# Performance work log

Hardware: AMD Instinct MI355X
Metric: run time of the kernel (lower is better)

Reference implementation:

```python
import jax, jax.numpy as jnp
import numpy as np

QLEN, MLEN, BSZ = 1024, 1024, 2
D_MODEL, N_HEAD, D_HEAD, D_INNER = 1024, 16, 64, 4096
KLEN = QLEN + MLEN
RLEN = KLEN + QLEN
EPS = 1e-12
SCALE = 1.0 / np.sqrt(D_HEAD).astype(np.float32)
STD = 0.02


def gelu(x):
    # OpenAI-GPT tanh-approx gelu used by XLNet
    return 0.5 * x * (1.0 + jnp.tanh(np.sqrt(2.0 / np.pi) * (x + 0.044715 * x ** 3)))


def layer_norm(x, g, b):
    m = jnp.mean(x, axis=-1, keepdims=True)
    v = jnp.mean((x - m) ** 2, axis=-1, keepdims=True)
    return (x - m) * jax.lax.rsqrt(v + EPS) * g + b


def rel_shift(x, klen):
    # x: [qlen, rlen, bsz, n_head] -> [qlen, klen, bsz, n_head]
    q, r, b, n = x.shape
    x = jnp.reshape(x, (r, q, b, n))[1:]
    x = jnp.reshape(x, (q, r - 1, b, n))[:, :klen]
    return x


def setup_inputs() -> dict:
    key = jax.random.key(0)
    ks = jax.random.split(key, 16)
    h = jax.random.normal(ks[0], (QLEN, BSZ, D_MODEL), jnp.float32)
    mems = jax.random.normal(ks[1], (MLEN, BSZ, D_MODEL), jnp.float32)
    r = jax.random.normal(ks[2], (RLEN, BSZ, D_MODEL), jnp.float32)
    # segment one-hot: 1 if query and key segments differ (XLNet convention)
    qseg = jax.random.randint(ks[3], (QLEN, BSZ), 0, 2)
    kseg = jax.random.randint(ks[4], (KLEN, BSZ), 0, 2)
    seg_mat = jax.nn.one_hot((qseg[:, None, :] != kseg[None, :, :]).astype(jnp.int32), 2, dtype=jnp.float32)  # [q,k,b,2]
    # causal mask with mems: query i may attend to key j <= i + MLEN
    i = jnp.arange(QLEN)[:, None]
    j = jnp.arange(KLEN)[None, :]
    attn_mask = (j > i + MLEN).astype(jnp.float32)[:, :, None, None]  # [q,k,1,1]
    wq = jax.random.normal(ks[5], (D_MODEL, N_HEAD, D_HEAD), jnp.float32) * STD
    wk = jax.random.normal(ks[6], (D_MODEL, N_HEAD, D_HEAD), jnp.float32) * STD
    wv = jax.random.normal(ks[7], (D_MODEL, N_HEAD, D_HEAD), jnp.float32) * STD
    wo = jax.random.normal(ks[8], (D_MODEL, N_HEAD, D_HEAD), jnp.float32) * STD
    wr = jax.random.normal(ks[9], (D_MODEL, N_HEAD, D_HEAD), jnp.float32) * STD
    r_w_bias = jnp.zeros((N_HEAD, D_HEAD), jnp.float32)
    r_r_bias = jnp.zeros((N_HEAD, D_HEAD), jnp.float32)
    r_s_bias = jnp.zeros((N_HEAD, D_HEAD), jnp.float32)
    seg_embed = jax.random.normal(ks[10], (2, N_HEAD, D_HEAD), jnp.float32) * STD
    ln_attn_g = jnp.ones((D_MODEL,), jnp.float32)
    ln_attn_b = jnp.zeros((D_MODEL,), jnp.float32)
    w1 = jax.random.normal(ks[11], (D_MODEL, D_INNER), jnp.float32) * STD
    b1 = jnp.zeros((D_INNER,), jnp.float32)
    w2 = jax.random.normal(ks[12], (D_INNER, D_MODEL), jnp.float32) * STD
    b2 = jnp.zeros((D_MODEL,), jnp.float32)
    ln_ff_g = jnp.ones((D_MODEL,), jnp.float32)
    ln_ff_b = jnp.zeros((D_MODEL,), jnp.float32)
    return dict(h=h, mems=mems, r=r, seg_mat=seg_mat, attn_mask=attn_mask,
                wq=wq, wk=wk, wv=wv, wo=wo, wr=wr,
                r_w_bias=r_w_bias, r_r_bias=r_r_bias, r_s_bias=r_s_bias, seg_embed=seg_embed,
                ln_attn_g=ln_attn_g, ln_attn_b=ln_attn_b,
                w1=w1, b1=b1, w2=w2, b2=b2, ln_ff_g=ln_ff_g, ln_ff_b=ln_ff_b)


def reference(h, mems, r, seg_mat, attn_mask, wq, wk, wv, wo, wr,
              r_w_bias, r_r_bias, r_s_bias, seg_embed,
              ln_attn_g, ln_attn_b, w1, b1, w2, b2, ln_ff_g, ln_ff_b):
    # content-stream XLNet relative attention (g=None path) + FFN
    cat = jnp.concatenate([mems, h], axis=0)            # [klen,b,h]
    q_h = jnp.einsum('ibh,hnd->ibnd', h, wq)
    k_h = jnp.einsum('ibh,hnd->ibnd', cat, wk)
    v_h = jnp.einsum('ibh,hnd->ibnd', cat, wv)
    k_r = jnp.einsum('ibh,hnd->ibnd', r, wr)
    ac = jnp.einsum('ibnd,jbnd->ijbn', q_h + r_w_bias, k_h)
    bd = jnp.einsum('ibnd,jbnd->ijbn', q_h + r_r_bias, k_r)
    bd = rel_shift(bd, KLEN)
    ef = jnp.einsum('ibnd,snd->ibns', q_h + r_s_bias, seg_embed)
    ef = jnp.einsum('ijbs,ibns->ijbn', seg_mat, ef)
    attn_score = (ac + bd + ef) * SCALE - 1e30 * attn_mask
    attn_prob = jax.nn.softmax(attn_score, axis=1)
    attn_vec = jnp.einsum('ijbn,jbnd->ibnd', attn_prob, v_h)
    attn_out = jnp.einsum('ibnd,hnd->ibh', attn_vec, wo) + h
    out_h = layer_norm(attn_out, ln_attn_g, ln_attn_b)
    ff = gelu(out_h @ w1 + b1) @ w2 + b2
    return layer_norm(ff + out_h, ln_ff_g, ln_ff_b)
```

## Files before the change

### kernel.cpp

```cpp
#include <hip/hip_runtime.h>
#include <hip/hip_bf16.h>


#define QLEN 1024
#define MLEN 1024
#define DM 1024
#define NH 16
#define DH 64
#define DI 4096
#define KLEN 2048
#define RLEN 3072

typedef __attribute__((ext_vector_type(8))) short s16x8;
typedef __attribute__((ext_vector_type(4))) float f32x4;
typedef unsigned short us;

__device__ __forceinline__ float bf2f(us u) {
    union { unsigned int i; float f; } x; x.i = ((unsigned int)u) << 16; return x.f;
}
__device__ __forceinline__ us f2bf(float f) {
    union { float f; unsigned int i; } x; x.f = f;
    return (us)((x.i + 0x7fffu + ((x.i >> 16) & 1u)) >> 16);
}
__device__ __forceinline__ void gload16(const void* g, void* lds) {
    __builtin_amdgcn_global_load_lds(
        (const __attribute__((address_space(1))) unsigned int*)g,
        (__attribute__((address_space(3))) unsigned int*)lds, 16, 0, 0);
}

template<bool ISMAX>
__device__ __forceinline__ float block_reduce(float v, float* red, int t) {
    #pragma unroll
    for (int off = 32; off > 0; off >>= 1) {
        float o = __shfl_down(v, off);
        v = ISMAX ? fmaxf(v, o) : (v + o);
    }
    if ((t & 63) == 0) red[t >> 6] = v;
    __syncthreads();
    if (t == 0) {
        float s = red[0];
        #pragma unroll
        for (int w = 1; w < 4; ++w) s = ISMAX ? fmaxf(s, red[w]) : (s + red[w]);
        red[4] = s;
    }
    __syncthreads();
    return red[4];
}

__global__ __launch_bounds__(256) void prep_k(
    const float* __restrict__ mems, const float* __restrict__ h,
    const float* __restrict__ r, const float* __restrict__ wo,
    const float* __restrict__ wq, const float* __restrict__ wk,
    const float* __restrict__ wv, const float* __restrict__ wr,
    const float* __restrict__ w1, const float* __restrict__ w2,
    const float* __restrict__ seg,
    us* __restrict__ cat_bf, us* __restrict__ r_bf, us* __restrict__ wo_b,
    us* __restrict__ wqkv_t, us* __restrict__ wr_t,
    us* __restrict__ w1_t, us* __restrict__ w2_t, us* __restrict__ ksb)
{
    __shared__ us tbuf[64][65];
    int bid = blockIdx.x;
    const int tid = threadIdx.x;
    if (bid < 5632) {
        int t = bid * 256 + tid;
        const float* src; us* dst; int off;
        if (t < 262144)       { src = mems; dst = cat_bf;           off = t; }
        else if (t < 524288)  { src = h;    dst = cat_bf + 2097152; off = t - 262144; }
        else if (t < 1310720) { src = r;    dst = r_bf;             off = t - 524288; }
        else                  { src = wo;   dst = wo_b;             off = t - 1310720; }
        const float4* p = (const float4*)src + 2 * (size_t)off;
        float4 a = p[0], b = p[1];
        us o[8] = { f2bf(a.x), f2bf(a.y), f2bf(a.z), f2bf(a.w),
                    f2bf(b.x), f2bf(b.y), f2bf(b.z), f2bf(b.w) };
        *((uint4*)dst + off) = *(const uint4*)o;
        return;
    }
    bid -= 5632;
    if (bid >= 3072) {
        int t = (bid - 3072) * 256 + tid;
        int bb = t >> 11, j = t & 2047;
        ksb[t] = f2bf(seg[(size_t)j * 4 + bb * 2 + 1]);
        return;
    }
    const float* in; us* out; int R, C, c0, r0;
    if (bid < 1024) {
        int z = bid >> 8, u = bid & 255;
        in  = (z == 0) ? wq : (z == 1) ? wk : (z == 2) ? wv : wr;
        out = (z < 3) ? (wqkv_t + (size_t)z * 1048576) : wr_t;
        R = 1024; C = 1024; c0 = (u & 15) * 64; r0 = (u >> 4) * 64;
    } else if (bid < 2048) {
        int u = bid - 1024;
        in = w1; out = w1_t; R = 1024; C = 4096;
        c0 = (u & 63) * 64; r0 = (u >> 6) * 64;
    } else {
        int u = bid - 2048;
        in = w2; out = w2_t; R = 4096; C = 1024;
        c0 = (u & 15) * 64; r0 = (u >> 4) * 64;
    }
    #pragma unroll
    for (int u = 0; u < 16; ++u) {
        int idx = tid + 256 * u;
        int rr = idx >> 6, cc = idx & 63;
        tbuf[cc][rr] = f2bf(in[(size_t)(r0 + rr) * C + c0 + cc]);
    }
    __syncthreads();
    #pragma unroll
    for (int u = 0; u < 16; ++u) {
        int idx = tid + 256 * u;
        int rr = idx >> 6, cc = idx & 63;
        out[(size_t)(c0 + rr) * R + r0 + cc] = tbuf[rr][cc];
    }
}

__device__ __forceinline__ int offe(int r, int c) {
    return ((r >> 4) * 2 + (c >> 5)) * 512 + (r & 15) * 32 + ((c & 31) ^ ((r & 8) ? 16 : 0));
}

template<int EPI>
__device__ __forceinline__ void gemm8_core(
    const us* __restrict__ A, const us* __restrict__ Bt,
    const float* __restrict__ bias, void* __restrict__ Cout,
    int N, int K, int kbeg, size_t zoff, bool zfirst,
    int bx, int by, us* __restrict__ As8, us* __restrict__ Bs8)
{
    const int tid = threadIdx.x;
    const int w = tid >> 6, l = tid & 63;
    const int lm = l & 15, lg = l >> 4;
    const int wm = w >> 2, wn = w & 3;
    const int m0 = by * 256, n0 = bx * 256;

    int srow[2], scol[2];
    #pragma unroll
    for (int u = 0; u < 2; ++u) {
        int sub = w * 2 + u;
        srow[u] = (sub >> 1) * 16 + (l >> 2);
        scol[u] = (sub & 1) * 32 + (((l & 3) * 8) ^ ((l & 32) ? 16 : 0));
    }

    auto stagePart = [&](int kt1, int P, int db) {
        const us* src = (P < 2) ? (A + (size_t)(m0 + P * 128) * K)
                                : (Bt + (size_t)(n0 + (P - 2) * 128) * K);
        us* dst = ((P < 2) ? As8 : Bs8) + (db * 2 + (P & 1)) * 8192;
        int kc = kbeg + kt1 * 64;
        #pragma unroll
        for (int u = 0; u < 2; ++u)
            gload16(src + (size_t)srow[u] * K + kc + scol[u], dst + (w * 2 + u) * 512);
    };

    f32x4 acc[8][4] = {};
    s16x8 rA0[4][2], rA1[4][2], rB[2][2];

    stagePart(0, 0, 0); stagePart(0, 1, 0); stagePart(0, 2, 0); stagePart(0, 3, 0);

    for (int kt = 0; kt < 16; ++kt) {
        const int d = kt & 1;
        asm volatile("s_waitcnt vmcnt(0)" ::: "memory");
        __builtin_amdgcn_s_barrier();
        asm volatile("" ::: "memory");
        const bool hn = (kt + 1 < 16);
        const us* Ab = As8 + (d * 2 + wm) * 8192;
        const us* Bb = Bs8 + (d * 2 + (wn >> 1)) * 8192;

        if (hn) stagePart(kt + 1, 0, d ^ 1);
        #pragma unroll
        for (int mf2 = 0; mf2 < 4; ++mf2)
            #pragma unroll
            for (int kk = 0; kk < 2; ++kk)
                rA0[mf2][kk] = *(const s16x8*)&Ab[offe(mf2 * 16 + lm, kk * 32 + lg * 8)];
        #pragma unroll
        for (int nf2 = 0; nf2 < 2; ++nf2)
            #pragma unroll
            for (int kk = 0; kk < 2; ++kk)
                rB[nf2][kk] = *(const s16x8*)&Bb[offe((wn & 1) * 64 + nf2 * 16 + lm, kk * 32 + lg * 8)];
        __builtin_amdgcn_s_setprio(1);
        #pragma unroll
        for (int mf2 = 0; mf2 < 4; ++mf2)
            #pragma unroll
            for (int nf2 = 0; nf2 < 2; ++nf2)
                #pragma unroll
                for (int kk = 0; kk < 2; ++kk)
                    acc[mf2][nf2] = __builtin_amdgcn_mfma_f32_16x16x32_bf16(
                        rA0[mf2][kk], rB[nf2][kk], acc[mf2][nf2], 0, 0, 0);
        __builtin_amdgcn_s_setprio(0);

        if (hn) stagePart(kt + 1, 1, d ^ 1);
        #pragma unroll
        for (int mf2 = 0; mf2 < 4; ++mf2)
            #pragma unroll
            for (int kk = 0; kk < 2; ++kk)
                rA1[mf2][kk] = *(const s16x8*)&Ab[offe(64 + mf2 * 16 + lm, kk * 32 + lg * 8)];
        __builtin_amdgcn_s_setprio(1);
        #pragma unroll
        for (int mf2 = 0; mf2 < 4; ++mf2)
            #pragma unroll
            for (int nf2 = 0; nf2 < 2; ++nf2)
                #pragma unroll
                for (int kk = 0; kk < 2; ++kk)
                    acc[4 + mf2][nf2] = __builtin_amdgcn_mfma_f32_16x16x32_bf16(
                        rA1[mf2][kk], rB[nf2][kk], acc[4 + mf2][nf2], 0, 0, 0);
        __builtin_amdgcn_s_setprio(0);

        if (hn) stagePart(kt + 1, 2, d ^ 1);
        #pragma unroll
        for (int nf2 = 0; nf2 < 2; ++nf2)
            #pragma unroll
            for (int kk = 0; kk < 2; ++kk)
                rB[nf2][kk] = *(const s16x8*)&Bb[offe((wn & 1) * 64 + (2 + nf2) * 16 + lm, kk * 32 + lg * 8)];
        __builtin_amdgcn_s_setprio(1);
        #pragma unroll
        for (int mf2 = 0; mf2 < 4; ++mf2)
            #pragma unroll
            for (int nf2 = 0; nf2 < 2; ++nf2)
                #pragma unroll
                for (int kk = 0; kk < 2; ++kk)
                    acc[4 + mf2][2 + nf2] = __builtin_amdgcn_mfma_f32_16x16x32_bf16(
                        rA1[mf2][kk], rB[nf2][kk], acc[4 + mf2][2 + nf2], 0, 0, 0);
        __builtin_amdgcn_s_setprio(0);

        if (hn) stagePart(kt + 1, 3, d ^ 1);
        __builtin_amdgcn_s_setprio(1);
        #pragma unroll
        for (int mf2 = 0; mf2 < 4; ++mf2)
            #pragma unroll
            for (int nf2 = 0; nf2 < 2; ++nf2)
                #pragma unroll
                for (int kk = 0; kk < 2; ++kk)
                    acc[mf2][2 + nf2] = __builtin_amdgcn_mfma_f32_16x16x32_bf16(
                        rA0[mf2][kk], rB[nf2][kk], acc[mf2][2 + nf2], 0, 0, 0);
        __builtin_amdgcn_s_setprio(0);
    }

    #pragma unroll
    for (int mf = 0; mf < 8; ++mf) {
        #pragma unroll
        for (int nf = 0; nf < 4; ++nf) {
            #pragma unroll
            for (int rr = 0; rr < 4; ++rr) {
                int row = m0 + wm * 128 + mf * 16 + lg * 4 + rr;
                int col = n0 + wn * 64 + nf * 16 + lm;
                float v = acc[mf][nf][rr];
                if (EPI == 3) {
                    int s = row >> 1, bb = row & 1, nn = col >> 6, dd = col & 63;
                    if (s >= 1) {
                        int g = (s - 1) >> 4, lmw = (s - 1) & 15;
                        int ks2 = dd >> 5, lg2 = (dd >> 3) & 3, e2 = dd & 7;
                        ((us*)Cout)[((((size_t)(bb * 16 + nn)) * 144 + g) * 2 + ks2) * 512
                                    + (lg2 * 16 + lmw) * 8 + e2] = f2bf(v);
                    }
                } else {
                    int which = col >> 10;
                    int nn = (col >> 6) & 15, dd = col & 63, bb = row & 1;
                    us val = f2bf(v);
                    us* base = (us*)Cout;
                    if (which == 0) {
                        if (row >= 2048)
                            base[(((size_t)(bb * 16 + nn)) * 1024 + ((row - 2048) >> 1)) * 64 + dd] = val;
                    } else if (which == 1) {
                        int j = row >> 1;
                        int jt = j >> 6, ff = (j >> 4) & 3, lmw = j & 15;
                        int ks2 = dd >> 5, lg2 = (dd >> 3) & 3, e2 = dd & 7;
                        (base + 2097152)[((((size_t)(bb * 16 + nn)) * 32 + jt) * 8 + ff * 2 + ks2) * 512
                                         + (lg2 * 16 + lmw) * 8 + e2] = val;
                    } else {
                        int j = row >> 1;
                        int jt = j >> 6, ks2 = (j >> 5) & 1, lg2 = (j >> 3) & 3, e2 = j & 7;
                        int df = dd >> 4, lmw = dd & 15;
                        (base + 6291456)[((((size_t)(bb * 16 + nn)) * 32 + jt) * 8 + df * 2 + ks2) * 512
                                         + (lg2 * 16 + lmw) * 8 + e2] = val;
                    }
                }
            }
        }
    }
}

__global__ __launch_bounds__(512) void proj8_k(
    const us* __restrict__ cat_bf, const us* __restrict__ wqkv_t,
    const us* __restrict__ r_bf, const us* __restrict__ wr_t,
    us* __restrict__ qkv_out, us* __restrict__ krf_out)
{
    __shared__ __align__(16) us As8[2 * 2 * 8192];
    __shared__ __align__(16) us Bs8[2 * 2 * 8192];
    int bid = blockIdx.x;
    if (bid < 192) {
        int swz = (bid & 7) * 24 + (bid >> 3);
        gemm8_core<4>(cat_bf, wqkv_t, nullptr, qkv_out, 3072, 1024, 0,
                      0, true, swz % 12, swz / 12, As8, Bs8);
    } else {
        int idx = bid - 192;
        gemm8_core<3>(r_bf, wr_t, nullptr, krf_out, 1024, 1024, 0,
                      0, true, idx & 3, idx >> 2, As8, Bs8);
    }
}

template<int TM, int EPI>
__device__ __forceinline__ void gemm_core(
    const us* __restrict__ A, const us* __restrict__ Bt,
    const float* __restrict__ bias, void* __restrict__ Cout,
    int N, int K, int kbeg, int kchunk, size_t zoff, bool zfirst,
    int bx, int by, us* __restrict__ As, us* __restrict__ Bs)
{
    constexpr int MF = TM / 32;
    constexpr int AISS = TM / 64;
    const int tid = threadIdx.x;
    const int w = tid >> 6, l = tid & 63;
    const int lm = l & 15, lg = l >> 4;
    const int m0 = by * TM, n0 = bx * 128;
    const int wr = (w >> 1) * (TM / 2), wc = (w & 1) * 64;
    const int nt = kchunk / 32;

    f32x4 acc[MF][4] = {};

    auto stage = [&](int buf, int k0) {
        #pragma unroll
        for (int u = 0; u < AISS; ++u) {
            int c = (u * 4 + w) * 64 + l;
            int row = c & (TM - 1), kc = c >> (TM == 128 ? 7 : 6);
            gload16(A + (size_t)(m0 + row) * K + k0 + kc * 8,
                    As + buf * (TM * 32) + (u * 4 + w) * 512);
        }
        #pragma unroll
        for (int u = 0; u < 2; ++u) {
            int c = (u * 4 + w) * 64 + l;
            int row = c & 127, kc = c >> 7;
            gload16(Bt + (size_t)(n0 + row) * K + k0 + kc * 8,
                    Bs + buf * 4096 + (u * 4 + w) * 512);
        }
    };

    stage(0, kbeg);
    int cur = 0;
    for (int t = 0; t < nt; ++t) {
        asm volatile("s_waitcnt vmcnt(0)" ::: "memory");
        __builtin_amdgcn_s_barrier();
        asm volatile("" ::: "memory");
        if (t + 1 < nt) stage(cur ^ 1, kbeg + (t + 1) * 32);

        s16x8 af[MF], bfr[4];
        #pragma unroll
        for (int mf = 0; mf < MF; ++mf)
            af[mf] = *(const s16x8*)&As[cur * (TM * 32) + (lg * TM + wr + mf * 16 + lm) * 8];
        #pragma unroll
        for (int nf = 0; nf < 4; ++nf)
            bfr[nf] = *(const s16x8*)&Bs[cur * 4096 + (lg * 128 + wc + nf * 16 + lm) * 8];
        #pragma unroll
        for (int mf = 0; mf < MF; ++mf)
            #pragma unroll
            for (int nf = 0; nf < 4; ++nf)
                acc[mf][nf] = __builtin_amdgcn_mfma_f32_16x16x32_bf16(
                    af[mf], bfr[nf], acc[mf][nf], 0, 0, 0);
        cur ^= 1;
    }

    #pragma unroll
    for (int mf = 0; mf < MF; ++mf) {
        #pragma unroll
        for (int nf = 0; nf < 4; ++nf) {
            #pragma unroll
            for (int rr = 0; rr < 4; ++rr) {
                int row = m0 + wr + mf * 16 + lg * 4 + rr;
                int col = n0 + wc + nf * 16 + lm;
                float v = acc[mf][nf][rr];
                if (EPI == 1 || (EPI == 2 && zfirst)) v += bias[col];
                if (EPI == 1) {
                    float targ = 0.7978845608028654f * (v + 0.044715f * v * v * v);
                    v = 0.5f * v * (1.0f + tanhf(targ));
                    ((us*)Cout)[(size_t)row * N + col] = f2bf(v);
                } else {
                    ((float*)Cout + zoff)[(size_t)row * N + col] = v;
                }
            }
        }
    }
}

template<int TM, int EPI>
__global__ __launch_bounds__(256) void gemm2(
    const us* __restrict__ A, const us* __restrict__ Bt,
    const float* __restrict__ bias, void* __restrict__ Cout,
    int N, int K, int kchunk, size_t zstride)
{
    __shared__ us As[2 * TM * 32];
    __shared__ us Bs[2 * 128 * 32];
    int lin = blockIdx.y * gridDim.x + blockIdx.x;
    int nwg = gridDim.x * gridDim.y;
    int swz = (lin & 7) * (nwg >> 3) + (lin >> 3);
    int bx = swz % gridDim.x, by = swz / gridDim.x;
    gemm_core<TM, EPI>(A, Bt, bias, Cout, N, K, blockIdx.z * kchunk, kchunk,
                       (size_t)blockIdx.z * zstride, blockIdx.z == 0, bx, by, As, Bs);
}

__global__ __launch_bounds__(256) void attn11_k(
    const us* __restrict__ qb, const us* __restrict__ kfr, const us* __restrict__ vfr,
    const us* __restrict__ krf, const us* __restrict__ ksb,
    const float* __restrict__ rwb, const float* __restrict__ rrb,
    const float* __restrict__ rsb, const float* __restrict__ se,
    const float* __restrict__ seg,
    float* __restrict__ po, float* __restrict__ pm, float* __restrict__ pl)
{
    __shared__ float G_lds[4 * 80 * 20];
    __shared__ us P_lds[4 * 16 * 64];
    __shared__ us KS_lds[2048];
    __shared__ float Qx_lds[64][2];

    const int tid = threadIdx.x;
    const int w = tid >> 6, l = tid & 63;
    const int lm = l & 15, lg = l >> 4;
    int lin = blockIdx.x;
    const int half = lin >> 9;
    const int i0t = (lin >> 5) & 15;
    const int bn = lin & 31;
    const int i0 = i0t * 64;
    const int b = bn >> 4, n = bn & 15;
    const int i = i0 + w * 16 + lm;

    const float SC = 0.125f * 1.44269504088896340736f;

    const us* kbase = kfr + (size_t)bn * 131072;
    const us* vbase = vfr + (size_t)bn * 131072;
    const us* krbase = krf + (size_t)bn * 147456;

    gload16(ksb + b * KLEN + (w * 64 + l) * 8, &KS_lds[w * 512]);
    {
        const us* qrow = qb + ((size_t)bn * QLEN + i0 + l) * DH;
        s16x8 qv8[8];
        #pragma unroll
        for (int c = 0; c < 8; ++c) qv8[c] = *(const s16x8*)(qrow + c * 8);
        float e0 = 0.f, e1 = 0.f;
        #pragma unroll
        for (int c = 0; c < 8; ++c)
            #pragma unroll
            for (int e = 0; e < 8; ++e) {
                int d = c * 8 + e;
                float qv = bf2f((us)qv8[c][e]) + rsb[n * DH + d];
                e0 = fmaf(qv, se[(0 * NH + n) * DH + d], e0);
                e1 = fmaf(qv, se[(1 * NH + n) * DH + d], e1);
            }
        float qsI = seg[(size_t)(i0 + l) * 8192 + b * 2 + 1];
        float qs0 = seg[b * 2 + 1];
        float qs = (qsI != qs0) ? 1.f : 0.f;
        float ed = e1 - e0;
        if (w == 0) {
            Qx_lds[l][0] = (e0 + qs * ed) * SC;
            Qx_lds[l][1] = ed * (1.f - 2.f * qs) * SC;
        }
    }
    asm volatile("s_waitcnt vmcnt(0)" ::: "memory");
    __syncthreads();

    s16x8 qwf[2], qrf[2], qxf;
    {
        const us* qrow = qb + ((size_t)bn * QLEN + i) * DH;
        #pragma unroll
        for (int ks = 0; ks < 2; ++ks) {
            s16x8 v = *(const s16x8*)(qrow + ks * 32 + lg * 8);
            #pragma unroll
            for (int e = 0; e < 8; ++e) {
                int d = ks * 32 + lg * 8 + e;
                float f = bf2f((us)v[e]);
                qwf[ks][e] = (short)f2bf((f + rwb[n * DH + d]) * SC);
                qrf[ks][e] = (short)f2bf((f + rrb[n * DH + d]) * SC);
            }
        }
        #pragma unroll
        for (int e = 0; e < 8; ++e) qxf[e] = 0;
        if (lg == 0) {
            qxf[0] = (short)f2bf(Qx_lds[w * 16 + lm][0]);
            qxf[1] = (short)f2bf(Qx_lds[w * 16 + lm][1]);
        }
    }

    int njt = ((i0 + 63 + MLEN) >> 6) + 1;
    if (njt > 32) njt = 32;
    const int nj0 = (njt + 1) >> 1;
    const int jbeg = half ? nj0 : 0;
    const int jend = half ? njt : nj0;
    const int gq = 63 - (i0 >> 4) - w;

    f32x4 of[4] = {{0,0,0,0},{0,0,0,0},{0,0,0,0},{0,0,0,0}};
    float M = -3.0e38f, L = 0.f;
    float* gw = &G_lds[w * 1600];
    us* pw = &P_lds[w * 1024];

    for (int jt = jbeg; jt < jend; ++jt) {
        const int j0 = jt * 64;

        s16x8 kf[4][2], vf[4][2];
        #pragma unroll
        for (int f = 0; f < 4; ++f) {
            #pragma unroll
            for (int ks = 0; ks < 2; ++ks) {
                kf[f][ks] = *(const s16x8*)(kbase + (size_t)(((jt * 4 + f) * 2 + ks) * 64 + l) * 8);
                vf[f][ks] = *(const s16x8*)(vbase + (size_t)(((jt * 4 + f) * 2 + ks) * 64 + l) * 8);
            }
        }

        __builtin_amdgcn_s_setprio(1);
        #pragma unroll
        for (int pf = 0; pf < 5; ++pf) {
            int g = gq + 4 * jt + pf;
            f32x4 gacc = {0, 0, 0, 0};
            #pragma unroll
            for (int ks = 0; ks < 2; ++ks) {
                s16x8 a = *(const s16x8*)(krbase + (size_t)((g * 2 + ks) * 64 + l) * 8);
                gacc = __builtin_amdgcn_mfma_f32_16x16x32_bf16(a, qrf[ks], gacc, 0, 0, 0);
            }
            #pragma unroll
            for (int rr = 0; rr < 4; ++rr)
                gw[(pf * 16 + lg * 4 + rr) * 20 + lm] = gacc[rr];
        }
        f32x4 sf[4];
        #pragma unroll
        for (int f = 0; f < 4; ++f) {
            f32x4 cfr = {0, 0, 0, 0};
            cfr = __builtin_amdgcn_mfma_f32_16x16x32_bf16(kf[f][0], qwf[0], cfr, 0, 0, 0);
            cfr = __builtin_amdgcn_mfma_f32_16x16x32_bf16(kf[f][1], qwf[1], cfr, 0, 0, 0);
            s16x8 aext;
            #pragma unroll
            for (int e = 0; e < 8; ++e) aext[e] = 0;
            if (lg == 0) {
                aext[0] = (short)0x3F80;
                aext[1] = (short)KS_lds[j0 + f * 16 + lm];
            }
            cfr = __builtin_amdgcn_mfma_f32_16x16x32_bf16(aext, qxf, cfr, 0, 0, 0);
            sf[f] = cfr;
        }
        __builtin_amdgcn_s_setprio(0);

        float sv[16];
        #pragma unroll
        for (int f = 0; f < 4; ++f)
            #pragma unroll
            for (int rr = 0; rr < 4; ++rr) {
                int jl = f * 16 + lg * 4 + rr;
                sv[f * 4 + rr] = sf[f][rr] + gw[(jl + 15 - lm) * 20 + lm];
            }
        if (j0 + 63 > i0 + w * 16 + MLEN) {
            #pragma unroll
            for (int f = 0; f < 4; ++f)
                #pragma unroll
                for (int rr = 0; rr < 4; ++rr) {
                    int jl = f * 16 + lg * 4 + rr;
                    if (j0 + jl > i + MLEN) sv[f * 4 + rr] = -1.0e30f;
                }
        }
        float tmax = sv[0];
        #pragma unroll
        for (int u = 1; u < 16; ++u) tmax = fmaxf(tmax, sv[u]);
        tmax = fmaxf(tmax, __shfl_xor(tmax, 16));
        tmax = fmaxf(tmax, __shfl_xor(tmax, 32));
        float Mnew = fmaxf(M, tmax);
        float scale;
        asm("v_exp_f32 %0, %1" : "=v"(scale) : "v"(M - Mnew));
        float psum = 0.f;
        unsigned int pk[8];
        #pragma unroll
        for (int f = 0; f < 4; ++f) {
            #pragma unroll
            for (int rp = 0; rp < 2; ++rp) {
                float p0, p1;
                asm("v_exp_f32 %0, %1" : "=v"(p0) : "v"(sv[f * 4 + rp * 2] - Mnew));
                asm("v_exp_f32 %0, %1" : "=v"(p1) : "v"(sv[f * 4 + rp * 2 + 1] - Mnew));
                psum += p0 + p1;
                unsigned int pkv;
                asm("v_cvt_pk_bf16_f32 %0, %1, %2" : "=v"(pkv) : "v"(p0), "v"(p1));
                pk[f * 2 + rp] = pkv;
            }
        }
        psum += __shfl_xor(psum, 16);
        psum += __shfl_xor(psum, 32);
        L = L * scale + psum;
        M = Mnew;
        float rs4[4];
        #pragma unroll
        for (int rr = 0; rr < 4; ++rr)
            rs4[rr] = __shfl(scale, (l & 48) | (lg * 4 + rr));
        #pragma unroll
        for (int df = 0; df < 4; ++df)
            #pragma unroll
            for (int rr = 0; rr < 4; ++rr)
                of[df][rr] *= rs4[rr];
        #pragma unroll
        for (int f = 0; f < 4; ++f) {
            #pragma unroll
            for (int rp = 0; rp < 2; ++rp) {
                int jl2 = f * 16 + lg * 4 + rp * 2;
                *(unsigned int*)&pw[lm * 64 + (((jl2 * 2) ^ ((lm & 7) << 4)) >> 1)] = pk[f * 2 + rp];
            }
        }
        __builtin_amdgcn_s_setprio(1);
        #pragma unroll
        for (int ks = 0; ks < 2; ++ks) {
            s16x8 pa = *(const s16x8*)&pw[lm * 64 + (((ks * 64 + lg * 16) ^ ((lm & 7) << 4)) >> 1)];
            #pragma unroll
            for (int df = 0; df < 4; ++df)
                of[df] = __builtin_amdgcn_mfma_f32_16x16x32_bf16(pa, vf[df][ks], of[df], 0, 0, 0);
        }
        __builtin_amdgcn_s_setprio(0);
    }

    const int pidx = (half * 16 + i0t) * 32 + bn;
    float rl4[4], rm4[4];
    #pragma unroll
    for (int rr = 0; rr < 4; ++rr) {
        rl4[rr] = __shfl(L, (l & 48) | (lg * 4 + rr));
        rm4[rr] = __shfl(M, (l & 48) | (lg * 4 + rr));
    }
    #pragma unroll
    for (int df = 0; df < 4; ++df) {
        #pragma unroll
        for (int rr = 0; rr < 4; ++rr) {
            int rloc = w * 16 + lg * 4 + rr;
            po[((size_t)pidx * 64 + rloc) * 64 + df * 16 + lm] = of[df][rr];
        }
    }
    if (lm == 0) {
        #pragma unroll
        for (int rr = 0; rr < 4; ++rr) {
            int rloc = w * 16 + lg * 4 + rr;
            pm[pidx * 64 + rloc] = rm4[rr];
            pl[pidx * 64 + rloc] = rl4[rr];
        }
    }
}

__global__ __launch_bounds__(256) void avcomb_k(
    const float* __restrict__ po, const float* __restrict__ pm,
    const float* __restrict__ pl, us* __restrict__ av)
{
    const int avrow = blockIdx.x;
    const int t = threadIdx.x;
    const int i = avrow >> 1, b = avrow & 1;
    const int i0t = i >> 6, rl = i & 63;
    const int col0 = t * 4;
    const int n = col0 >> 6, d0 = col0 & 63;
    const int bn = b * 16 + n;
    const int p0 = (0 + i0t) * 32 + bn;
    const int p1 = (16 + i0t) * 32 + bn;
    float M0 = pm[p0 * 64 + rl], M1 = pm[p1 * 64 + rl];
    float L0 = pl[p0 * 64 + rl], L1 = pl[p1 * 64 + rl];
    float Mx = fmaxf(M0, M1);
    float s0, s1;
    asm("v_exp_f32 %0, %1" : "=v"(s0) : "v"(M0 - Mx));
    asm("v_exp_f32 %0, %1" : "=v"(s1) : "v"(M1 - Mx));
    float inv = 1.0f / (L0 * s0 + L1 * s1);
    float4 o0 = *(const float4*)&po[((size_t)p0 * 64 + rl) * 64 + d0];
    float4 o1 = *(const float4*)&po[((size_t)p1 * 64 + rl) * 64 + d0];
    us o[4] = { f2bf((o0.x * s0 + o1.x * s1) * inv),
                f2bf((o0.y * s0 + o1.y * s1) * inv),
                f2bf((o0.z * s0 + o1.z * s1) * inv),
                f2bf((o0.w * s0 + o1.w * s1) * inv) };
    *(unsigned long long*)&av[(size_t)avrow * 1024 + col0] = *(const unsigned long long*)o;
}

template<int NSUM, bool RESBF, bool OUTBF>
__global__ __launch_bounds__(256) void ln_k(
    const float* __restrict__ a, const void* __restrict__ resid,
    const float* __restrict__ g, const float* __restrict__ bb,
    void* __restrict__ out)
{
    __shared__ float xs[DM];
    __shared__ float red[5];
    const int r = blockIdx.x;
    const int t = threadIdx.x;
    float lsum = 0.f;
    #pragma unroll
    for (int u = 0; u < 4; ++u) {
        int hdx = t + 256 * u;
        float x = RESBF ? bf2f(((const us*)resid)[(size_t)r * DM + hdx])
                        : ((const float*)resid)[(size_t)r * DM + hdx];
        #pragma unroll
        for (int s = 0; s < NSUM; ++s)
            x += a[(size_t)s * 2097152 + (size_t)r * DM + hdx];
        xs[hdx] = x;
        lsum += x;
    }
    float m = block_reduce<false>(lsum, red, t) * (1.0f / DM);
    float lv = 0.f;
    #pragma unroll
    for (int u = 0; u < 4; ++u) {
        int hdx = t + 256 * u;
        float dd = xs[hdx] - m;
        lv += dd * dd;
    }
    float var = block_reduce<false>(lv, red, t) * (1.0f / DM);
    float rs = rsqrtf(var + 1e-12f);
    #pragma unroll
    for (int u = 0; u < 4; ++u) {
        int hdx = t + 256 * u;
        float y = (xs[hdx] - m) * rs * g[hdx] + bb[hdx];
        if (OUTBF) ((us*)out)[(size_t)r * DM + hdx] = f2bf(y);
        else       ((float*)out)[(size_t)r * DM + hdx] = y;
    }
}

extern "C" void kernel_launch(void* const* d_in, const int* in_sizes, int n_in,
                              void* d_out, int out_size, void* d_ws, size_t ws_size,
                              hipStream_t stream) {
    const float* h         = (const float*)d_in[0];
    const float* mems      = (const float*)d_in[1];
    const float* r         = (const float*)d_in[2];
    const float* seg_mat   = (const float*)d_in[3];
    const float* wq        = (const float*)d_in[5];
    const float* wk        = (const float*)d_in[6];
    const float* wv        = (const float*)d_in[7];
    const float* wo        = (const float*)d_in[8];
    const float* wr        = (const float*)d_in[9];
    const float* rwb       = (const float*)d_in[10];
    const float* rrb       = (const float*)d_in[11];
    const float* rsb       = (const float*)d_in[12];
    const float* seg_embed = (const float*)d_in[13];
    const float* ln_g      = (const float*)d_in[14];
    const float* ln_b      = (const float*)d_in[15];
    const float* w1        = (const float*)d_in[16];
    const float* b1        = (const float*)d_in[17];
    const float* w2        = (const float*)d_in[18];
    const float* b2        = (const float*)d_in[19];
    const float* lf_g      = (const float*)d_in[20];
    const float* lf_b      = (const float*)d_in[21];
    float* out = (float*)d_out;
    char* W = (char*)d_ws;
    const size_t MB = 1ull << 20;

    us*    cat_bf = (us*)(W);
    us*    r_bf   = (us*)(W + 8  * MB);
    us*    wqkv_t = (us*)(W + 20 * MB);
    us*    wr_t   = (us*)(W + 26 * MB);
    us*    wo_b   = (us*)(W + 28 * MB);
    us*    w1_t   = (us*)(W + 30 * MB);
    us*    w2_t   = (us*)(W + 38 * MB);
    us*    q_bf   = (us*)(W + 46 * MB);
    us*    kfrag  = q_bf + 2097152;
    us*    vfrag  = q_bf + 6291456;
    us*    krf    = (us*)(W + 66 * MB);
    us*    av_bf  = (us*)(W + 78 * MB);
    us*    ks_bf  = (us*)(W + 82 * MB);
    us*    oh_bf  = (us*)(W + 83 * MB);
    float* po     = (float*)(W + 8 * MB);
    float* pm     = (float*)(W + 24 * MB);
    float* pl     = (float*)(W + 24 * MB + 512 * 1024);
    float* ao     = (float*)(W + 8 * MB);
    us*    ff1_bf = (us*)(W + 46 * MB);
    float* ff2    = (float*)(W);

    dim3 blk(256);
    dim3 blk8(512);
    prep_k<<<dim3(8720), blk, 0, stream>>>(mems, h, r, wo, wq, wk, wv, wr, w1, w2, seg_mat,
                                           cat_bf, r_bf, wo_b, wqkv_t, wr_t, w1_t, w2_t, ks_bf);
    proj8_k<<<dim3(264), blk8, 0, stream>>>(cat_bf, wqkv_t, r_bf, wr_t, q_bf, krf);
    attn11_k<<<dim3(1024), blk, 0, stream>>>(q_bf, kfrag, vfrag, krf, ks_bf,
                                             rwb, rrb, rsb, seg_embed, seg_mat, po, pm, pl);
    avcomb_k<<<dim3(2048), blk, 0, stream>>>(po, pm, pl, av_bf);
    gemm2<64, 0><<<dim3(8, 32, 2), blk, 0, stream>>>(av_bf, wo_b, nullptr, ao, 1024, 1024, 512, 2097152);
    ln_k<2, false, true><<<dim3(2048), blk, 0, stream>>>(ao, h, ln_g, ln_b, oh_bf);
    gemm2<128, 1><<<dim3(32, 16), blk, 0, stream>>>(oh_bf, w1_t, b1, ff1_bf, 4096, 1024, 1024, 0);
    gemm2<64, 2><<<dim3(8, 32, 4), blk, 0, stream>>>(ff1_bf, w2_t, b2, ff2, 1024, 4096, 1024, 2097152);
    ln_k<4, true, false><<<dim3(2048), blk, 0, stream>>>(ff2, oh_bf, lf_g, lf_b, out);
}
```

Before: 307.1 us.

## Shrink projection GEMM tiles to 128x128 for more blocks and occupancy

Replaces the 256x256-tile projection GEMM with a 128x128-tile variant: 8 waves each compute a 64x32 sub-tile, shared memory is halved, and launch bounds ask for 4 blocks per CU. The grid grows from 264 to 1040 blocks, with new swizzles for both the QKV and the relative-key GEMMs. The aim is to fill the 256 CUs better than 264 large tiles did (about one wave of blocks with a ragged tail) and to raise occupancy for latency hiding. In exchange, each tile reuses its loads less, so global and LDS traffic per FLOP goes up.

```diff
diff --git a/kernel.cpp b/kernel.cpp
--- a/kernel.cpp
+++ b/kernel.cpp
@@ -117,127 +117,94 @@
 }
 
 template<int EPI>
-__device__ __forceinline__ void gemm8_core(
-    const us* __restrict__ A, const us* __restrict__ Bt,
-    const float* __restrict__ bias, void* __restrict__ Cout,
-    int N, int K, int kbeg, size_t zoff, bool zfirst,
-    int bx, int by, us* __restrict__ As8, us* __restrict__ Bs8)
+__device__ __forceinline__ void gemm8h_core(
+    const us* __restrict__ A, const us* __restrict__ Bt, void* __restrict__ Cout,
+    int N, int K, int bx, int by, us* __restrict__ As8, us* __restrict__ Bs8)
 {
     const int tid = threadIdx.x;
     const int w = tid >> 6, l = tid & 63;
     const int lm = l & 15, lg = l >> 4;
     const int wm = w >> 2, wn = w & 3;
-    const int m0 = by * 256, n0 = bx * 256;
+    const int m0 = by * 128, n0 = bx * 128;
 
     int srow[2], scol[2];
     #pragma unroll
     for (int u = 0; u < 2; ++u) {
-        int sub = w * 2 + u;
+        int sub = u * 8 + w;
         srow[u] = (sub >> 1) * 16 + (l >> 2);
         scol[u] = (sub & 1) * 32 + (((l & 3) * 8) ^ ((l & 32) ? 16 : 0));
     }
 
-    auto stagePart = [&](int kt1, int P, int db) {
-        const us* src = (P < 2) ? (A + (size_t)(m0 + P * 128) * K)
-                                : (Bt + (size_t)(n0 + (P - 2) * 128) * K);
-        us* dst = ((P < 2) ? As8 : Bs8) + (db * 2 + (P & 1)) * 8192;
-        int kc = kbeg + kt1 * 64;
-        #pragma unroll
-        for (int u = 0; u < 2; ++u)
-            gload16(src + (size_t)srow[u] * K + kc + scol[u], dst + (w * 2 + u) * 512);
+    auto stageHalf = [&](int kt1, bool isB, int u, int db) {
+        const us* src = isB ? (Bt + (size_t)n0 * K) : (A + (size_t)m0 * K);
+        us* dst = (isB ? Bs8 : As8) + db * 8192 + (u * 8 + w) * 512;
+        gload16(src + (size_t)srow[u] * K + kt1 * 64 + scol[u], dst);
     };
 
-    f32x4 acc[8][4] = {};
-    s16x8 rA0[4][2], rA1[4][2], rB[2][2];
-
-    stagePart(0, 0, 0); stagePart(0, 1, 0); stagePart(0, 2, 0); stagePart(0, 3, 0);
-
-    for (int kt = 0; kt < 16; ++kt) {
+    f32x4 acc[4][2] = {};
+    const int nkt = K / 64;
+
+    stageHalf(0, false, 0, 0); stageHalf(0, false, 1, 0);
+    stageHalf(0, true, 0, 0);  stageHalf(0, true, 1, 0);
+
+    for (int kt = 0; kt < nkt; ++kt) {
         const int d = kt & 1;
         asm volatile("s_waitcnt vmcnt(0)" ::: "memory");
         __builtin_amdgcn_s_barrier();
         asm volatile("" ::: "memory");
-        const bool hn = (kt + 1 < 16);
-        const us* Ab = As8 + (d * 2 + wm) * 8192;
-        const us* Bb = Bs8 + (d * 2 + (wn >> 1)) * 8192;
-
-        if (hn) stagePart(kt + 1, 0, d ^ 1);
-        #pragma unroll
-        for (int mf2 = 0; mf2 < 4; ++mf2)
+        const bool hn = (kt + 1 < nkt);
+        const us* Ab = As8 + d * 8192;
+        const us* Bb = Bs8 + d * 8192;
+
+        if (hn) { stageHalf(kt + 1, false, 0, d ^ 1); stageHalf(kt + 1, true, 0, d ^ 1); }
+        s16x8 rB[2][2], rA[2][2];
+        #pragma unroll
+        for (int nf = 0; nf < 2; ++nf)
             #pragma unroll
             for (int kk = 0; kk < 2; ++kk)
-                rA0[mf2][kk] = *(const s16x8*)&Ab[offe(mf2 * 16 + lm, kk * 32 + lg * 8)];
-        #pragma unroll
-        for (int nf2 = 0; nf2 < 2; ++nf2)
+                rB[nf][kk] = *(const s16x8*)&Bb[offe(wn * 32 + nf * 16 + lm, kk * 32 + lg * 8)];
+        #pragma unroll
+        for (int mf = 0; mf < 2; ++mf)
             #pragma unroll
             for (int kk = 0; kk < 2; ++kk)
-                rB[nf2][kk] = *(const s16x8*)&Bb[offe((wn & 1) * 64 + nf2 * 16 + lm, kk * 32 + lg * 8)];
+                rA[mf][kk] = *(const s16x8*)&Ab[offe(wm * 64 + mf * 16 + lm, kk * 32 + lg * 8)];
         __builtin_amdgcn_s_setprio(1);
         #pragma unroll
-        for (int mf2 = 0; mf2 < 4; ++mf2)
-            #pragma unroll
-            for (int nf2 = 0; nf2 < 2; ++nf2)
+        for (int mf = 0; mf < 2; ++mf)
+            #pragma unroll
+            for (int nf = 0; nf < 2; ++nf)
                 #pragma unroll
                 for (int kk = 0; kk < 2; ++kk)
-                    acc[mf2][nf2] = __builtin_amdgcn_mfma_f32_16x16x32_bf16(
-                        rA0[mf2][kk], rB[nf2][kk], acc[mf2][nf2], 0, 0, 0);
+                    acc[mf][nf] = __builtin_amdgcn_mfma_f32_16x16x32_bf16(
+                        rA[mf][kk], rB[nf][kk], acc[mf][nf], 0, 0, 0);
         __builtin_amdgcn_s_setprio(0);
 
-        if (hn) stagePart(kt + 1, 1, d ^ 1);
-        #pragma unroll
-        for (int mf2 = 0; mf2 < 4; ++mf2)
+        if (hn) { stageHalf(kt + 1, false, 1, d ^ 1); stageHalf(kt + 1, true, 1, d ^ 1); }
+        #pragma unroll
+        for (int mf = 0; mf < 2; ++mf)
             #pragma unroll
             for (int kk = 0; kk < 2; ++kk)
-                rA1[mf2][kk] = *(const s16x8*)&Ab[offe(64 + mf2 * 16 + lm, kk * 32 + lg * 8)];
+                rA[mf][kk] = *(const s16x8*)&Ab[offe(wm * 64 + (2 + mf) * 16 + lm, kk * 32 + lg * 8)];
         __builtin_amdgcn_s_setprio(1);
         #pragma unroll
-        for (int mf2 = 0; mf2 < 4; ++mf2)
-            #pragma unroll
-            for (int nf2 = 0; nf2 < 2; ++nf2)
+        for (int mf = 0; mf < 2; ++mf)
+            #pragma unroll
+            for (int nf = 0; nf < 2; ++nf)
                 #pragma unroll
                 for (int kk = 0; kk < 2; ++kk)
-                    acc[4 + mf2][nf2] = __builtin_amdgcn_mfma_f32_16x16x32_bf16(
-                        rA1[mf2][kk], rB[nf2][kk], acc[4 + mf2][nf2], 0, 0, 0);
+                    acc[2 + mf][nf] = __builtin_amdgcn_mfma_f32_16x16x32_bf16(
+                        rA[mf][kk], rB[nf][kk], acc[2 + mf][nf], 0, 0, 0);
         __builtin_amdgcn_s_setprio(0);
-
-        if (hn) stagePart(kt + 1, 2, d ^ 1);
-        #pragma unroll
-        for (int nf2 = 0; nf2 < 2; ++nf2)
-            #pragma unroll
-            for (int kk = 0; kk < 2; ++kk)
-                rB[nf2][kk] = *(const s16x8*)&Bb[offe((wn & 1) * 64 + (2 + nf2) * 16 + lm, kk * 32 + lg * 8)];
-        __builtin_amdgcn_s_setprio(1);
-        #pragma unroll
-        for (int mf2 = 0; mf2 < 4; ++mf2)
-            #pragma unroll
-            for (int nf2 = 0; nf2 < 2; ++nf2)
-                #pragma unroll
-                for (int kk = 0; kk < 2; ++kk)
-                    acc[4 + mf2][2 + nf2] = __builtin_amdgcn_mfma_f32_16x16x32_bf16(
-                        rA1[mf2][kk], rB[nf2][kk], acc[4 + mf2][2 + nf2], 0, 0, 0);
-        __builtin_amdgcn_s_setprio(0);
-
-        if (hn) stagePart(kt + 1, 3, d ^ 1);
-        __builtin_amdgcn_s_setprio(1);
-        #pragma unroll
-        for (int mf2 = 0; mf2 < 4; ++mf2)
-            #pragma unroll
-            for (int nf2 = 0; nf2 < 2; ++nf2)
-                #pragma unroll
-                for (int kk = 0; kk < 2; ++kk)
-                    acc[mf2][2 + nf2] = __builtin_amdgcn_mfma_f32_16x16x32_bf16(
-                        rA0[mf2][kk], rB[nf2][kk], acc[mf2][2 + nf2], 0, 0, 0);
-        __builtin_amdgcn_s_setprio(0);
-    }
-
-    #pragma unroll
-    for (int mf = 0; mf < 8; ++mf) {
-        #pragma unroll
-        for (int nf = 0; nf < 4; ++nf) {
+    }
+
+    #pragma unroll
+    for (int mf = 0; mf < 4; ++mf) {
+        #pragma unroll
+        for (int nf = 0; nf < 2; ++nf) {
             #pragma unroll
             for (int rr = 0; rr < 4; ++rr) {
-                int row = m0 + wm * 128 + mf * 16 + lg * 4 + rr;
-                int col = n0 + wn * 64 + nf * 16 + lm;
+                int row = m0 + wm * 64 + mf * 16 + lg * 4 + rr;
+                int col = n0 + wn * 32 + nf * 16 + lm;
                 float v = acc[mf][nf][rr];
                 if (EPI == 3) {
                     int s = row >> 1, bb = row & 1, nn = col >> 6, dd = col & 63;
@@ -274,22 +241,23 @@
     }
 }
 
-__global__ __launch_bounds__(512) void proj8_k(
+__global__ __launch_bounds__(512, 4) void proj8_k(
     const us* __restrict__ cat_bf, const us* __restrict__ wqkv_t,
     const us* __restrict__ r_bf, const us* __restrict__ wr_t,
     us* __restrict__ qkv_out, us* __restrict__ krf_out)
 {
-    __shared__ __align__(16) us As8[2 * 2 * 8192];
-    __shared__ __align__(16) us Bs8[2 * 2 * 8192];
+    __shared__ __align__(16) us As8[2 * 8192];
+    __shared__ __align__(16) us Bs8[2 * 8192];
     int bid = blockIdx.x;
-    if (bid < 192) {
-        int swz = (bid & 7) * 24 + (bid >> 3);
-        gemm8_core<4>(cat_bf, wqkv_t, nullptr, qkv_out, 3072, 1024, 0,
-                      0, true, swz % 12, swz / 12, As8, Bs8);
+    if (bid < 768) {
+        int swz = (bid & 7) * 96 + (bid >> 3);
+        gemm8h_core<4>(cat_bf, wqkv_t, qkv_out, 3072, 1024,
+                       swz % 24, swz / 24, As8, Bs8);
     } else {
-        int idx = bid - 192;
-        gemm8_core<3>(r_bf, wr_t, nullptr, krf_out, 1024, 1024, 0,
-                      0, true, idx & 3, idx >> 2, As8, Bs8);
+        int idx = bid - 768;
+        int swz = (idx & 7) * 34 + (idx >> 3);
+        gemm8h_core<3>(r_bf, wr_t, krf_out, 1024, 1024,
+                       swz % 8, swz / 8, As8, Bs8);
     }
 }
 
@@ -747,7 +715,7 @@
     dim3 blk8(512);
     prep_k<<<dim3(8720), blk, 0, stream>>>(mems, h, r, wo, wq, wk, wv, wr, w1, w2, seg_mat,
                                            cat_bf, r_bf, wo_b, wqkv_t, wr_t, w1_t, w2_t, ks_bf);
-    proj8_k<<<dim3(264), blk8, 0, stream>>>(cat_bf, wqkv_t, r_bf, wr_t, q_bf, krf);
+    proj8_k<<<dim3(1040), blk8, 0, stream>>>(cat_bf, wqkv_t, r_bf, wr_t, q_bf, krf);
     attn11_k<<<dim3(1024), blk, 0, stream>>>(q_bf, kfrag, vfrag, krf, ks_bf,
                                              rwb, rrb, rsb, seg_embed, seg_mat, po, pm, pl);
     avcomb_k<<<dim3(2048), blk, 0, stream>>>(po, pm, pl, av_bf);
```

New measurement: 290.5 us. 1.06x faster.
